# Optimization experiments

Hardware: AMD Instinct MI355X
Metric: run time of the kernel (lower is better)

The kernel has to match this reference:

```python
import jax, jax.numpy as jnp
import numpy as np

N, D0, D1, HID, OUT = 4096, 256, 128, 64, 16
R, M, K, PROJ = 3, 2, 2, 128  # meta-path rels, same-type rels, schema rels, attn hidden


def setup_inputs() -> dict:
    key = jax.random.key(0)
    ks = jax.random.split(key, 24)
    g = lambda i, shape, s: jax.random.normal(ks[i], shape, jnp.float32) * s
    return {
        "features0": g(0, (N, D0), 1.0),
        "features1": g(1, (N, D1), 1.0),
        # row-scale adjacencies so aggregated features stay O(1)
        "adj_same": jax.random.uniform(ks[2], (M, N, N), jnp.float32) / N,
        "adj_meta": jax.random.uniform(ks[3], (R, N, N), jnp.float32) / N,
        "adj_schema": jax.random.uniform(ks[4], (K, N, N), jnp.float32) / N,
        "Wm0": g(5, (D0, HID), D0 ** -0.5), "bm0": jnp.zeros((HID,), jnp.float32),
        "Wm1": g(6, (D1, HID), D1 ** -0.5), "bm1": jnp.zeros((HID,), jnp.float32),
        "Wa": g(7, (HID, PROJ), HID ** -0.5), "ba": jnp.zeros((PROJ,), jnp.float32),
        "qa": g(8, (PROJ,), PROJ ** -0.5),
        "ws": g(9, (HID, 1), HID ** -0.5),
        "Wc1": g(10, (HID, PROJ), HID ** -0.5), "bc1": jnp.zeros((PROJ,), jnp.float32),
        "wc2": g(11, (PROJ, 1), PROJ ** -0.5),
        "Wt1": g(12, (HID, PROJ), HID ** -0.5), "bt1": jnp.zeros((PROJ,), jnp.float32),
        "wt2": g(13, (PROJ, 1), PROJ ** -0.5),
        "Wp": g(14, (HID, OUT), HID ** -0.5), "bp": jnp.zeros((OUT,), jnp.float32),
    }


def reference(features0, features1, adj_same, adj_meta, adj_schema,
              Wm0, bm0, Wm1, bm1, Wa, ba, qa, ws, Wc1, bc1, wc2,
              Wt1, bt1, wt2, Wp, bp):
    # per-type feature mapping: tanh(Linear(x))
    h0 = jnp.tanh(features0 @ Wm0 + bm0)  # [N, HID]
    h1 = jnp.tanh(features1 @ Wm1 + bm1)  # [N, HID]

    # --- Dif_Classes_AGG: meta-path aggregation + semantic attention over R relations ---
    hr = jnp.tanh(jnp.einsum('rij,jd->rid', adj_meta, h0))        # [R, N, HID]
    s = jnp.mean(jnp.tanh(hr @ Wa + ba) @ qa, axis=1)             # [R]
    beta_r = jax.nn.softmax(s)                                    # [R]
    relation_agg = jnp.einsum('r,rnd->nd', beta_r, hr)            # [N, HID]

    # --- Weight_Schema: schema-matrix aggregation with per-node softmax over K ---
    zk = jnp.einsum('kij,jd->kid', adj_schema, h1)                # [K, N, HID]
    beta_k = jax.nn.softmax(jnp.squeeze(zk @ ws, -1), axis=0)     # [K, N]
    item_classes_agg = jnp.einsum('kn,knd->nd', beta_k, zk)       # [N, HID]

    # --- Classes_Relation_AGG: same-type (item-item) aggregation over M relations ---
    ym = jnp.tanh(jnp.einsum('mij,jd->mid', adj_same, item_classes_agg))  # [M, N, HID]
    wm = jnp.squeeze(jnp.tanh(ym @ Wc1 + bc1) @ wc2, -1)          # [M, N]
    beta_m = jax.nn.softmax(wm, axis=0)                           # [M, N]
    item_item = jnp.einsum('mn,mnd->nd', beta_m, ym)              # [N, HID]

    # --- AggAttention over the two module outputs ---
    Hs = jnp.stack([relation_agg, item_item], axis=1)             # [N, 2, HID]
    wt = jnp.squeeze(jnp.tanh(Hs @ Wt1 + bt1) @ wt2, -1)          # [N, 2]
    beta_t = jax.nn.softmax(wt, axis=1)[..., None]                # [N, 2, 1]
    H = jnp.sum(beta_t * Hs, axis=1)                              # [N, HID]

    return (H @ Wp + bp, H)
```

## Files before the change

kernel.cpp:

```cpp
#include <hip/hip_runtime.h>

#define NODES 4096

typedef float f32x4 __attribute__((ext_vector_type(4)));
typedef __bf16 bf16x8 __attribute__((ext_vector_type(8)));
typedef __bf16 bf16x4 __attribute__((ext_vector_type(4)));
typedef unsigned short u16x8 __attribute__((ext_vector_type(8)));
typedef unsigned short u16x4 __attribute__((ext_vector_type(4)));

__device__ __forceinline__ unsigned short f2bf(float x) {
    unsigned u = __builtin_bit_cast(unsigned, x);
    return (unsigned short)((u + 0x7fffu + ((u >> 16) & 1u)) >> 16);
}

__global__ __launch_bounds__(256) void prep_h(
    const float* __restrict__ f0, const float* __restrict__ f1,
    const float* __restrict__ Wm0, const float* __restrict__ bm0,
    const float* __restrict__ Wm1, const float* __restrict__ bm1,
    unsigned short* __restrict__ hB0, unsigned short* __restrict__ hB1)
{
    const int d = threadIdx.x & 63;
    int n = blockIdx.x * 4 + (threadIdx.x >> 6);
    n = __builtin_amdgcn_readfirstlane(n);
    const float* r0 = f0 + (size_t)n * 256;
    float a0 = bm0[d];
#pragma unroll 8
    for (int k = 0; k < 256; ++k) a0 = fmaf(r0[k], Wm0[k * 64 + d], a0);
    hB0[((size_t)(n >> 3)) * 512 + d * 8 + (n & 7)] = f2bf(tanhf(a0));
    const float* r1 = f1 + (size_t)n * 128;
    float a1 = bm1[d];
#pragma unroll 8
    for (int k = 0; k < 128; ++k) a1 = fmaf(r1[k], Wm1[k * 64 + d], a1);
    hB1[((size_t)(n >> 3)) * 512 + d * 8 + (n & 7)] = f2bf(tanhf(a1));
}

__global__ __launch_bounds__(256) void adj_gemm(
    const float* __restrict__ A0, const float* __restrict__ A1,
    const float* __restrict__ A2, const float* __restrict__ A3,
    const float* __restrict__ A4,
    const unsigned short* __restrict__ hBa, const unsigned short* __restrict__ hBb,
    int split, float* __restrict__ outBase)
{
    __shared__ __align__(16) char smem[2][16384];

    const int job = blockIdx.y;
    const float* adj = job == 0 ? A0 : job == 1 ? A1 : job == 2 ? A2 : job == 3 ? A3 : A4;
    const unsigned short* hB = (job < split) ? hBa : hBb;

    const int group = blockIdx.x >> 1;
    const int kh = blockIdx.x & 1;
    const int n0 = group * 64;
    const int kbeg = kh * 2048;

    const int t = threadIdx.x;
    const int lane = t & 63, w = t >> 6;
    const int fr = lane & 15, fg = lane >> 4;

    const char* aSrcT = (const char*)adj
        + ((size_t)(n0 + (t >> 4)) * NODES + kbeg) * 4 + (size_t)(t & 15) * 16;
    const char* bSrcT = (const char*)hB + ((size_t)(kbeg >> 3)) * 1024 + (size_t)t * 16;

    int aw[4];
#pragma unroll
    for (int g = 0; g < 4; ++g) {
        const int r = g * 16 + (t >> 4);
        aw[g] = r * 128 + ((((t & 15) * 8)) ^ ((r & 7) << 4));
    }
    int bw[2];
#pragma unroll
    for (int j = 0; j < 2; ++j) {
        const int L = (t + 256 * j) * 16;
        const int kb = L >> 10;
        const int d = (L >> 4) & 63;
        bw[j] = 8192 + kb * 1024 + ((d * 16) ^ (kb << 4));
    }

    f32x4 RAa0, RAa1, RAa2, RAa3, RAb0, RAb1;
    f32x4 RBa0, RBa1, RBa2, RBa3, RBb0, RBb1;

#define LOADX(P, c) {                                                        \
    P##a0 = *(const f32x4*)(aSrcT + 0 * 262144 + (c) * 256);                 \
    P##a1 = *(const f32x4*)(aSrcT + 1 * 262144 + (c) * 256);                 \
    P##a2 = *(const f32x4*)(aSrcT + 2 * 262144 + (c) * 256);                 \
    P##a3 = *(const f32x4*)(aSrcT + 3 * 262144 + (c) * 256);                 \
    P##b0 = *(const f32x4*)(bSrcT + (c) * 8192);                             \
    P##b1 = *(const f32x4*)(bSrcT + 4096 + (c) * 8192); }

#define STOREX(P, buf) {                                                     \
    *(u16x4*)((buf) + aw[0]) = __builtin_bit_cast(u16x4, __builtin_convertvector(P##a0, bf16x4)); \
    *(u16x4*)((buf) + aw[1]) = __builtin_bit_cast(u16x4, __builtin_convertvector(P##a1, bf16x4)); \
    *(u16x4*)((buf) + aw[2]) = __builtin_bit_cast(u16x4, __builtin_convertvector(P##a2, bf16x4)); \
    *(u16x4*)((buf) + aw[3]) = __builtin_bit_cast(u16x4, __builtin_convertvector(P##a3, bf16x4)); \
    *(f32x4*)((buf) + bw[0]) = P##b0;                                        \
    *(f32x4*)((buf) + bw[1]) = P##b1; }

    f32x4 acc0 = {0.f,0.f,0.f,0.f}, acc1 = {0.f,0.f,0.f,0.f};
    f32x4 acc2 = {0.f,0.f,0.f,0.f}, acc3 = {0.f,0.f,0.f,0.f};

    const int arow = w * 16 + fr;
    const int aswz = (fr & 7) << 4;

#define COMPUTE(buf) {                                                       \
    _Pragma("unroll")                                                        \
    for (int ks = 0; ks < 2; ++ks) {                                         \
        u16x8 a16 = *(const u16x8*)((buf) + arow * 128 + ((ks * 64 + fg * 16) ^ aswz)); \
        bf16x8 af = __builtin_bit_cast(bf16x8, a16);                         \
        const int kb = ks * 4 + fg;                                          \
        u16x8 b0 = *(const u16x8*)((buf) + 8192 + kb * 1024 + (((0 * 16 + fr) * 16) ^ (kb << 4))); \
        acc0 = __builtin_amdgcn_mfma_f32_16x16x32_bf16(af, __builtin_bit_cast(bf16x8, b0), acc0, 0, 0, 0); \
        u16x8 b1 = *(const u16x8*)((buf) + 8192 + kb * 1024 + (((1 * 16 + fr) * 16) ^ (kb << 4))); \
        acc1 = __builtin_amdgcn_mfma_f32_16x16x32_bf16(af, __builtin_bit_cast(bf16x8, b1), acc1, 0, 0, 0); \
        u16x8 b2 = *(const u16x8*)((buf) + 8192 + kb * 1024 + (((2 * 16 + fr) * 16) ^ (kb << 4))); \
        acc2 = __builtin_amdgcn_mfma_f32_16x16x32_bf16(af, __builtin_bit_cast(bf16x8, b2), acc2, 0, 0, 0); \
        u16x8 b3 = *(const u16x8*)((buf) + 8192 + kb * 1024 + (((3 * 16 + fr) * 16) ^ (kb << 4))); \
        acc3 = __builtin_amdgcn_mfma_f32_16x16x32_bf16(af, __builtin_bit_cast(bf16x8, b3), acc3, 0, 0, 0); \
    } }

    LOADX(RA, 0);
    STOREX(RA, smem[0]);

    for (int c = 0; c < 32; c += 2) {
        LOADX(RB, c + 1);
        __syncthreads();
        COMPUTE(smem[0]);
        STOREX(RB, smem[1]);
        if (c + 2 < 32) LOADX(RA, c + 2);
        __syncthreads();
        COMPUTE(smem[1]);
        if (c + 2 < 32) STOREX(RA, smem[0]);
    }

#undef LOADX
#undef STOREX
#undef COMPUTE

    float* C = outBase + (size_t)job * (NODES * 64);
    float* Cw = C + (size_t)(n0 + w * 16 + fg * 4) * 64 + fr;
#pragma unroll
    for (int j = 0; j < 4; ++j) {
        atomicAdd(&Cw[j * 64 + 0],  acc0[j]);
        atomicAdd(&Cw[j * 64 + 16], acc1[j]);
        atomicAdd(&Cw[j * 64 + 32], acc2[j]);
        atomicAdd(&Cw[j * 64 + 48], acc3[j]);
    }
}

__global__ __launch_bounds__(128) void stage_c(
    const float* __restrict__ agg, const float* __restrict__ Wa,
    const float* __restrict__ ba, const float* __restrict__ qa,
    const float* __restrict__ wsv, float* __restrict__ sacc,
    unsigned short* __restrict__ iccB)
{
    const int n = blockIdx.x;
    const int p = threadIdx.x;
    __shared__ float rs[3][2];
    __shared__ float ru[2][2];
    __shared__ float th[3][64];

    const float* h0p = agg + (size_t)n * 64;
    const float* h1p = agg + ((size_t)NODES + n) * 64;
    const float* h2p = agg + ((size_t)2 * NODES + n) * 64;
    if (p < 64) {
        th[0][p] = tanhf(h0p[p]);
        th[1][p] = tanhf(h1p[p]);
        th[2][p] = tanhf(h2p[p]);
    }
    __syncthreads();
    float a0 = ba[p], a1 = a0, a2 = a0;
#pragma unroll 8
    for (int d = 0; d < 64; ++d) {
        float w = Wa[d * 128 + p];
        a0 = fmaf(th[0][d], w, a0);
        a1 = fmaf(th[1][d], w, a1);
        a2 = fmaf(th[2][d], w, a2);
    }
    float qv = qa[p];
    float v0 = tanhf(a0) * qv, v1 = tanhf(a1) * qv, v2 = tanhf(a2) * qv;

    const float* z0 = agg + ((size_t)3 * NODES + n) * 64;
    const float* z1 = agg + ((size_t)4 * NODES + n) * 64;
    float u0 = (p < 64) ? z0[p] * wsv[p] : 0.f;
    float u1 = (p < 64) ? z1[p] * wsv[p] : 0.f;

#pragma unroll
    for (int off = 32; off; off >>= 1) {
        v0 += __shfl_down(v0, off); v1 += __shfl_down(v1, off); v2 += __shfl_down(v2, off);
        u0 += __shfl_down(u0, off); u1 += __shfl_down(u1, off);
    }
    if ((p & 63) == 0) {
        int w = p >> 6;
        rs[0][w] = v0; rs[1][w] = v1; rs[2][w] = v2;
        ru[0][w] = u0; ru[1][w] = u1;
    }
    __syncthreads();
    if (p < 3) atomicAdd(&sacc[p], rs[p][0] + rs[p][1]);

    float U0 = ru[0][0] + ru[0][1];
    float U1 = ru[1][0] + ru[1][1];
    float mx = fmaxf(U0, U1);
    float e0 = expf(U0 - mx), e1 = expf(U1 - mx);
    float inv = 1.f / (e0 + e1);
    if (p < 64) {
        float icc = (e0 * z0[p] + e1 * z1[p]) * inv;
        iccB[((size_t)(n >> 3)) * 512 + p * 8 + (n & 7)] = f2bf(icc);
    }
}

__global__ __launch_bounds__(256) void finalize(
    const float* __restrict__ agg, const float* __restrict__ ym,
    const float* __restrict__ sacc,
    const float* __restrict__ Wc1, const float* __restrict__ bc1, const float* __restrict__ wc2,
    const float* __restrict__ Wt1, const float* __restrict__ bt1, const float* __restrict__ wt2,
    const float* __restrict__ Wp, const float* __restrict__ bp,
    float* __restrict__ out)
{
    __shared__ float sWc[64 * 128];
    __shared__ float sWp[64 * 16];
    __shared__ float sY0[2][64], sY1[2][64];
    __shared__ float sHs0[2][64], sHs1[2][64], sHv[2][64];
    __shared__ float rA[2][2], rB[2][2];

    const int t = threadIdx.x;
    for (int i = t; i < 64 * 128; i += 256) sWc[i] = Wc1[i];
    for (int i = t; i < 64 * 16; i += 256) sWp[i] = Wp[i];

    float s0 = sacc[0] * (1.f / NODES), s1 = sacc[1] * (1.f / NODES), s2 = sacc[2] * (1.f / NODES);
    float sm = fmaxf(s0, fmaxf(s1, s2));
    float b0 = expf(s0 - sm), b1 = expf(s1 - sm), b2 = expf(s2 - sm);
    float bi = 1.f / (b0 + b1 + b2);
    b0 *= bi; b1 *= bi; b2 *= bi;

    const int sub = t >> 7;
    const int p = t & 127;
    const int wiH = p >> 6;
    const float bcv = bc1[p], wcv = wc2[p], btv = bt1[p], wtv = wt2[p];
    __syncthreads();

    for (int it = 0; it < 8; ++it) {
        const int n = blockIdx.x * 16 + it * 2 + sub;
        if (p < 64) {
            const size_t NN64 = (size_t)NODES * 64;
            sY0[sub][p] = tanhf(ym[(size_t)n * 64 + p]);
            sY1[sub][p] = tanhf(ym[NN64 + (size_t)n * 64 + p]);
            sHs0[sub][p] = b0 * tanhf(agg[(size_t)n * 64 + p])
                         + b1 * tanhf(agg[((size_t)NODES + n) * 64 + p])
                         + b2 * tanhf(agg[((size_t)2 * NODES + n) * 64 + p]);
        }
        __syncthreads();
        float ac0 = bcv, ac1 = bcv;
#pragma unroll 8
        for (int d = 0; d < 64; ++d) {
            float w = sWc[d * 128 + p];
            ac0 = fmaf(sY0[sub][d], w, ac0);
            ac1 = fmaf(sY1[sub][d], w, ac1);
        }
        float v0 = tanhf(ac0) * wcv, v1 = tanhf(ac1) * wcv;
#pragma unroll
        for (int off = 32; off; off >>= 1) { v0 += __shfl_down(v0, off); v1 += __shfl_down(v1, off); }
        if ((p & 63) == 0) { rA[sub][wiH] = v0; rB[sub][wiH] = v1; }
        __syncthreads();
        float wm0 = rA[sub][0] + rA[sub][1];
        float wm1 = rB[sub][0] + rB[sub][1];
        float mm = fmaxf(wm0, wm1);
        float g0 = expf(wm0 - mm), g1 = expf(wm1 - mm);
        float gi = 1.f / (g0 + g1);
        g0 *= gi; g1 *= gi;
        if (p < 64) sHs1[sub][p] = g0 * sY0[sub][p] + g1 * sY1[sub][p];
        __syncthreads();

        float at0 = btv, at1 = btv;
#pragma unroll 8
        for (int d = 0; d < 64; ++d) {
            float w = Wt1[d * 128 + p];
            at0 = fmaf(sHs0[sub][d], w, at0);
            at1 = fmaf(sHs1[sub][d], w, at1);
        }
        float q0 = tanhf(at0) * wtv, q1 = tanhf(at1) * wtv;
#pragma unroll
        for (int off = 32; off; off >>= 1) { q0 += __shfl_down(q0, off); q1 += __shfl_down(q1, off); }
        if ((p & 63) == 0) { rA[sub][wiH] = q0; rB[sub][wiH] = q1; }
        __syncthreads();
        float t0 = rA[sub][0] + rA[sub][1];
        float t1 = rB[sub][0] + rB[sub][1];
        float tm = fmaxf(t0, t1);
        float c0 = expf(t0 - tm), c1 = expf(t1 - tm);
        float ci = 1.f / (c0 + c1);
        c0 *= ci; c1 *= ci;
        if (p < 64) {
            float H = c0 * sHs0[sub][p] + c1 * sHs1[sub][p];
            sHv[sub][p] = H;
            out[(size_t)NODES * 16 + (size_t)n * 64 + p] = H;
        }
        __syncthreads();
        if (p < 16) {
            float a = bp[p];
#pragma unroll 8
            for (int d = 0; d < 64; ++d) a = fmaf(sHv[sub][d], sWp[d * 16 + p], a);
            out[(size_t)n * 16 + p] = a;
        }
        __syncthreads();
    }
}

extern "C" void kernel_launch(void* const* d_in, const int* in_sizes, int n_in,
                              void* d_out, int out_size, void* d_ws, size_t ws_size,
                              hipStream_t stream)
{
    const float* f0   = (const float*)d_in[0];
    const float* f1   = (const float*)d_in[1];
    const float* adjS = (const float*)d_in[2];
    const float* adjM = (const float*)d_in[3];
    const float* adjK = (const float*)d_in[4];
    const float* Wm0  = (const float*)d_in[5];
    const float* bm0  = (const float*)d_in[6];
    const float* Wm1  = (const float*)d_in[7];
    const float* bm1  = (const float*)d_in[8];
    const float* Wa   = (const float*)d_in[9];
    const float* ba   = (const float*)d_in[10];
    const float* qa   = (const float*)d_in[11];
    const float* wsv  = (const float*)d_in[12];
    const float* Wc1  = (const float*)d_in[13];
    const float* bc1  = (const float*)d_in[14];
    const float* wc2  = (const float*)d_in[15];
    const float* Wt1  = (const float*)d_in[16];
    const float* bt1  = (const float*)d_in[17];
    const float* wt2  = (const float*)d_in[18];
    const float* Wp   = (const float*)d_in[19];
    const float* bpv  = (const float*)d_in[20];
    float* out = (float*)d_out;

    char* ws = (char*)d_ws;
    unsigned short* hB0  = (unsigned short*)(ws);
    unsigned short* hB1  = (unsigned short*)(ws + 524288);
    unsigned short* iccB = (unsigned short*)(ws + 1048576);
    float* agg           = (float*)(ws + 1572864);
    float* ym            = (float*)(ws + 6815744);
    float* sacc          = (float*)(ws + 8912896);

    hipMemsetAsync(agg, 0, 5 * 1048576, stream);
    hipMemsetAsync(ym, 0, 2 * 1048576, stream);
    hipMemsetAsync(sacc, 0, 64, stream);
    prep_h<<<dim3(1024), dim3(256), 0, stream>>>(f0, f1, Wm0, bm0, Wm1, bm1, hB0, hB1);

    const size_t NNs = (size_t)NODES * NODES;
    adj_gemm<<<dim3(128, 5), dim3(256), 0, stream>>>(
        adjM, adjM + NNs, adjM + 2 * NNs, adjK, adjK + NNs,
        hB0, hB1, 3, agg);
    stage_c<<<dim3(4096), dim3(128), 0, stream>>>(agg, Wa, ba, qa, wsv, sacc, iccB);
    adj_gemm<<<dim3(128, 2), dim3(256), 0, stream>>>(
        adjS, adjS + NNs, adjS, adjS, adjS,
        iccB, iccB, 5, ym);
    finalize<<<dim3(256), dim3(256), 0, stream>>>(
        agg, ym, sacc, Wc1, bc1, wc2, Wt1, bt1, wt2, Wp, bpv, out);
}
```

Measured before the change: 258.9 us.

## Pre-convert adjacency matrices to bf16 and run GEMMs on bf16 tiles

Adds a pass that converts all seven fp32 adjacency matrices to bf16 in workspace on every call. A new GEMM kernel then streams bf16 tiles, which halves the bytes each GEMM reads and removes the in-loop conversion. The second stage now splits K four ways to launch more blocks. The conversion pass adds a full fp32 read plus a bf16 write, so total memory traffic goes up. The path runs only when the workspace is large enough to hold the bf16 copies.

```diff
diff --git a/kernel.cpp b/kernel.cpp
--- a/kernel.cpp
+++ b/kernel.cpp
@@ -1,10 +1,11 @@
 #include <hip/hip_runtime.h>
 
 #define NODES 4096
+#define NN 16777216ULL
 
 typedef float f32x4 __attribute__((ext_vector_type(4)));
+typedef __bf16 bf16x4 __attribute__((ext_vector_type(4)));
 typedef __bf16 bf16x8 __attribute__((ext_vector_type(8)));
-typedef __bf16 bf16x4 __attribute__((ext_vector_type(4)));
 typedef unsigned short u16x8 __attribute__((ext_vector_type(8)));
 typedef unsigned short u16x4 __attribute__((ext_vector_type(4)));
 
@@ -34,7 +35,137 @@
     hB1[((size_t)(n >> 3)) * 512 + d * 8 + (n & 7)] = f2bf(tanhf(a1));
 }
 
-__global__ __launch_bounds__(256) void adj_gemm(
+__global__ __launch_bounds__(256) void cvt_adj(
+    const float* __restrict__ adjS, const float* __restrict__ adjM,
+    const float* __restrict__ adjK, unsigned short* __restrict__ dst)
+{
+    const int m = blockIdx.y;
+    const float* src = m < 3 ? adjM + (size_t)m * NN
+                     : m < 5 ? adjK + (size_t)(m - 3) * NN
+                             : adjS + (size_t)(m - 5) * NN;
+    unsigned short* d = dst + (size_t)m * NN;
+    const size_t base = (size_t)blockIdx.x * 16384 + (size_t)threadIdx.x * 4;
+#pragma unroll
+    for (int i = 0; i < 16; ++i) {
+        const size_t idx = base + (size_t)i * 1024;
+        f32x4 v = *(const f32x4*)(src + idx);
+        u16x4 o = { f2bf(v[0]), f2bf(v[1]), f2bf(v[2]), f2bf(v[3]) };
+        *(u16x4*)(d + idx) = o;
+    }
+}
+
+__global__ __launch_bounds__(256) void adj_gemm_b16(
+    const unsigned short* __restrict__ adjB, int slotBase,
+    const unsigned short* __restrict__ hBa, const unsigned short* __restrict__ hBb,
+    int split, float* __restrict__ outBase, int khBits)
+{
+    __shared__ __align__(16) char smem[2][32768];
+
+    const int job = blockIdx.y;
+    const unsigned short* adj = adjB + (size_t)(slotBase + job) * NN;
+    const unsigned short* hB = (job < split) ? hBa : hBb;
+
+    const int group = blockIdx.x >> khBits;
+    const int kh = blockIdx.x & ((1 << khBits) - 1);
+    const int n0 = group * 64;
+    const int klen = NODES >> khBits;
+    const int kbeg = kh * klen;
+    const int nc = klen >> 7;
+
+    const int t = threadIdx.x;
+    const int lane = t & 63, w = t >> 6;
+    const int fr = lane & 15, fg = lane >> 4;
+
+    const char* aSrcT = (const char*)adj
+        + ((size_t)(n0 + (t >> 4)) * NODES + kbeg) * 2 + (size_t)(t & 15) * 16;
+    const char* bSrcT = (const char*)hB + ((size_t)(kbeg >> 3)) * 1024 + (size_t)t * 16;
+
+    int aw[4];
+#pragma unroll
+    for (int g = 0; g < 4; ++g) {
+        const int r = (t >> 4) + g * 16;
+        aw[g] = r * 256 + (((t & 15) * 16) ^ ((r & 7) << 4));
+    }
+    int bw[4];
+#pragma unroll
+    for (int j = 0; j < 4; ++j) {
+        const int L = (t + 256 * j) * 16;
+        const int kb = L >> 10;
+        const int d = (L >> 4) & 63;
+        bw[j] = 16384 + kb * 1024 + ((d * 16) ^ (kb << 4));
+    }
+
+    u16x8 RAa0, RAa1, RAa2, RAa3, RAb0, RAb1, RAb2, RAb3;
+    u16x8 RBa0, RBa1, RBa2, RBa3, RBb0, RBb1, RBb2, RBb3;
+
+#define LOADXB(P, c) {                                                       \
+    P##a0 = *(const u16x8*)(aSrcT + 0 * 131072 + (size_t)(c) * 256);         \
+    P##a1 = *(const u16x8*)(aSrcT + 1 * 131072 + (size_t)(c) * 256);         \
+    P##a2 = *(const u16x8*)(aSrcT + 2 * 131072 + (size_t)(c) * 256);         \
+    P##a3 = *(const u16x8*)(aSrcT + 3 * 131072 + (size_t)(c) * 256);         \
+    P##b0 = *(const u16x8*)(bSrcT + 0 * 4096 + (size_t)(c) * 16384);         \
+    P##b1 = *(const u16x8*)(bSrcT + 1 * 4096 + (size_t)(c) * 16384);         \
+    P##b2 = *(const u16x8*)(bSrcT + 2 * 4096 + (size_t)(c) * 16384);         \
+    P##b3 = *(const u16x8*)(bSrcT + 3 * 4096 + (size_t)(c) * 16384); }
+
+#define STOREXB(P, buf) {                                                    \
+    *(u16x8*)((buf) + aw[0]) = P##a0;  *(u16x8*)((buf) + aw[1]) = P##a1;     \
+    *(u16x8*)((buf) + aw[2]) = P##a2;  *(u16x8*)((buf) + aw[3]) = P##a3;     \
+    *(u16x8*)((buf) + bw[0]) = P##b0;  *(u16x8*)((buf) + bw[1]) = P##b1;     \
+    *(u16x8*)((buf) + bw[2]) = P##b2;  *(u16x8*)((buf) + bw[3]) = P##b3; }
+
+    f32x4 acc0 = {0.f,0.f,0.f,0.f}, acc1 = {0.f,0.f,0.f,0.f};
+    f32x4 acc2 = {0.f,0.f,0.f,0.f}, acc3 = {0.f,0.f,0.f,0.f};
+
+    const int arow = w * 16 + fr;
+    const int aswz = (fr & 7) << 4;
+
+#define COMPUTEB(buf) {                                                      \
+    _Pragma("unroll")                                                        \
+    for (int ks = 0; ks < 4; ++ks) {                                         \
+        u16x8 a16 = *(const u16x8*)((buf) + arow * 256 + ((ks * 64 + fg * 16) ^ aswz)); \
+        bf16x8 af = __builtin_bit_cast(bf16x8, a16);                         \
+        const int kb = ks * 4 + fg;                                          \
+        u16x8 b0 = *(const u16x8*)((buf) + 16384 + kb * 1024 + (((0 * 16 + fr) * 16) ^ (kb << 4))); \
+        acc0 = __builtin_amdgcn_mfma_f32_16x16x32_bf16(af, __builtin_bit_cast(bf16x8, b0), acc0, 0, 0, 0); \
+        u16x8 b1 = *(const u16x8*)((buf) + 16384 + kb * 1024 + (((1 * 16 + fr) * 16) ^ (kb << 4))); \
+        acc1 = __builtin_amdgcn_mfma_f32_16x16x32_bf16(af, __builtin_bit_cast(bf16x8, b1), acc1, 0, 0, 0); \
+        u16x8 b2 = *(const u16x8*)((buf) + 16384 + kb * 1024 + (((2 * 16 + fr) * 16) ^ (kb << 4))); \
+        acc2 = __builtin_amdgcn_mfma_f32_16x16x32_bf16(af, __builtin_bit_cast(bf16x8, b2), acc2, 0, 0, 0); \
+        u16x8 b3 = *(const u16x8*)((buf) + 16384 + kb * 1024 + (((3 * 16 + fr) * 16) ^ (kb << 4))); \
+        acc3 = __builtin_amdgcn_mfma_f32_16x16x32_bf16(af, __builtin_bit_cast(bf16x8, b3), acc3, 0, 0, 0); \
+    } }
+
+    LOADXB(RA, 0);
+    STOREXB(RA, smem[0]);
+
+    for (int c = 0; c < nc; c += 2) {
+        LOADXB(RB, c + 1);
+        __syncthreads();
+        COMPUTEB(smem[0]);
+        STOREXB(RB, smem[1]);
+        if (c + 2 < nc) LOADXB(RA, c + 2);
+        __syncthreads();
+        COMPUTEB(smem[1]);
+        if (c + 2 < nc) STOREXB(RA, smem[0]);
+    }
+
+#undef LOADXB
+#undef STOREXB
+#undef COMPUTEB
+
+    float* C = outBase + (size_t)job * (NODES * 64);
+    float* Cw = C + (size_t)(n0 + w * 16 + fg * 4) * 64 + fr;
+#pragma unroll
+    for (int j = 0; j < 4; ++j) {
+        atomicAdd(&Cw[j * 64 + 0],  acc0[j]);
+        atomicAdd(&Cw[j * 64 + 16], acc1[j]);
+        atomicAdd(&Cw[j * 64 + 32], acc2[j]);
+        atomicAdd(&Cw[j * 64 + 48], acc3[j]);
+    }
+}
+
+__global__ __launch_bounds__(256) void adj_gemm_f32(
     const float* __restrict__ A0, const float* __restrict__ A1,
     const float* __restrict__ A2, const float* __restrict__ A3,
     const float* __restrict__ A4,
@@ -336,20 +467,30 @@
     float* agg           = (float*)(ws + 1572864);
     float* ym            = (float*)(ws + 6815744);
     float* sacc          = (float*)(ws + 8912896);
-
-    hipMemsetAsync(agg, 0, 5 * 1048576, stream);
-    hipMemsetAsync(ym, 0, 2 * 1048576, stream);
+    unsigned short* adjB = (unsigned short*)(ws + 8913920);
+    const bool useCvt = ws_size >= (8913920ULL + 7ULL * NN * 2ULL);
+
+    hipMemsetAsync(agg, 0, 7 * 1048576, stream);
     hipMemsetAsync(sacc, 0, 64, stream);
     prep_h<<<dim3(1024), dim3(256), 0, stream>>>(f0, f1, Wm0, bm0, Wm1, bm1, hB0, hB1);
 
-    const size_t NNs = (size_t)NODES * NODES;
-    adj_gemm<<<dim3(128, 5), dim3(256), 0, stream>>>(
-        adjM, adjM + NNs, adjM + 2 * NNs, adjK, adjK + NNs,
-        hB0, hB1, 3, agg);
-    stage_c<<<dim3(4096), dim3(128), 0, stream>>>(agg, Wa, ba, qa, wsv, sacc, iccB);
-    adj_gemm<<<dim3(128, 2), dim3(256), 0, stream>>>(
-        adjS, adjS + NNs, adjS, adjS, adjS,
-        iccB, iccB, 5, ym);
+    if (useCvt) {
+        cvt_adj<<<dim3(1024, 7), dim3(256), 0, stream>>>(adjS, adjM, adjK, adjB);
+        adj_gemm_b16<<<dim3(128, 5), dim3(256), 0, stream>>>(
+            adjB, 0, hB0, hB1, 3, agg, 1);
+        stage_c<<<dim3(4096), dim3(128), 0, stream>>>(agg, Wa, ba, qa, wsv, sacc, iccB);
+        adj_gemm_b16<<<dim3(256, 2), dim3(256), 0, stream>>>(
+            adjB, 5, iccB, iccB, 5, ym, 2);
+    } else {
+        const size_t NNs = (size_t)NODES * NODES;
+        adj_gemm_f32<<<dim3(128, 5), dim3(256), 0, stream>>>(
+            adjM, adjM + NNs, adjM + 2 * NNs, adjK, adjK + NNs,
+            hB0, hB1, 3, agg);
+        stage_c<<<dim3(4096), dim3(128), 0, stream>>>(agg, Wa, ba, qa, wsv, sacc, iccB);
+        adj_gemm_f32<<<dim3(128, 2), dim3(256), 0, stream>>>(
+            adjS, adjS + NNs, adjS, adjS, adjS,
+            iccB, iccB, 5, ym);
+    }
     finalize<<<dim3(256), dim3(256), 0, stream>>>(
         agg, ym, sacc, Wc1, bc1, wc2, Wt1, bt1, wt2, Wp, bpv, out);
 }
```

Measured after the change: 356.2 us. 1.38x slower.
